# Performance work log

Measured on AMD Instinct MI355X. Metric: run time of the kernel, lower is better.

## Reference

```python
import jax, jax.numpy as jnp
import numpy as np

S, B, E, D, W, V = 196, 64, 1024, 1800, 512, 32000


def setup_inputs() -> dict:
    key = jax.random.key(0)
    ks = jax.random.split(key, 16)
    def n(k, shape, s=0.02):
        return jax.random.normal(k, shape, jnp.float32) * s
    return {
        "E_tm1": jax.random.randint(ks[0], (B,), 0, V),
        "y_tm1": jax.random.normal(ks[1], (B, V), jnp.float32),
        "h": jax.random.normal(ks[2], (S, B, E), jnp.float32),
        "emb": n(ks[3], (V, W)),
        "W_ih": n(ks[4], (4 * D, W + E)), "b_ih": jnp.zeros((4 * D,), jnp.float32),
        "W_hh": n(ks[5], (4 * D, D)), "b_hh": jnp.zeros((4 * D,), jnp.float32),
        "W_out": n(ks[6], (V, W + D + E)), "b_out": jnp.zeros((V,), jnp.float32),
        "Wh1": n(ks[7], (D, E)), "bh1": jnp.zeros((D,), jnp.float32),
        "Wh2": n(ks[8], (D, D)), "bh2": jnp.zeros((D,), jnp.float32),
        "Wc1": n(ks[9], (D, E)), "bc1": jnp.zeros((D,), jnp.float32),
        "Wc2": n(ks[10], (D, D)), "bc2": jnp.zeros((D,), jnp.float32),
        "Wa1": n(ks[11], (D, D + E)), "ba1": jnp.zeros((D,), jnp.float32),
        "Wa2": n(ks[12], (1, D)), "ba2": jnp.zeros((1,), jnp.float32),
        "Wb": n(ks[13], (1, D)), "bb": jnp.zeros((1,), jnp.float32),
    }


def reference(E_tm1, y_tm1, h, emb, W_ih, b_ih, W_hh, b_hh, W_out, b_out,
              Wh1, bh1, Wh2, bh2, Wc1, bc1, Wc2, bc2, Wa1, ba1, Wa2, ba2, Wb, bb):
    # htilde_tm1 is None: init hidden/cell states from mean of encoder states
    h_avg = h.mean(axis=0)                                            # [B, E]
    h0 = jnp.maximum(h_avg @ Wh1.T + bh1, 0.0) @ Wh2.T + bh2          # [B, D]
    c0 = jnp.maximum(h_avg @ Wc1.T + bc1, 0.0) @ Wc2.T + bc2          # [B, D]
    # additive attention: concat(expanded queries, keys) -> MLP -> softmax over seq
    q = jnp.broadcast_to(h0[None], (S, B, D))                         # [S, B, D]
    ci = jnp.concatenate([q, h], axis=2)                              # [S, B, D+E]
    scores = jnp.maximum(ci @ Wa1.T + ba1, 0.0) @ Wa2.T + ba2          # [S, B, 1]
    aw = jax.nn.softmax(scores, axis=0)                                # softmax over seq_len
    ctx = jnp.einsum('sb,sbe->be', aw[..., 0], h)                      # [B, E]
    beta = jax.nn.sigmoid(h0 @ Wb.T + bb)                              # [B, 1] gating scalar
    ctx = ctx * beta
    # LSTM cell (torch gate order: i, f, g, o)
    x = jnp.concatenate([emb[E_tm1], ctx], axis=1)                     # [B, W+E]
    gates = x @ W_ih.T + b_ih + h0 @ W_hh.T + b_hh                     # [B, 4D]
    i, f, g, o = jnp.split(gates, 4, axis=1)
    c_t = jax.nn.sigmoid(f) * c0 + jax.nn.sigmoid(i) * jnp.tanh(g)
    h_t = jax.nn.sigmoid(o) * jnp.tanh(c_t)
    # deep output layer (dropout is identity in eval)
    y_emb = emb[jnp.argmax(y_tm1, axis=1)]                             # [B, W]
    logits = jnp.concatenate([h_t, y_emb, ctx], axis=1) @ W_out.T + b_out  # [B, V]
    return (logits, h_t, c_t, aw)
```

## Files before the change

kernel.cpp:

```cpp
#include <hip/hip_runtime.h>
#include <hip/hip_bf16.h>

typedef __bf16 bf16_t;
typedef __bf16 bf16x8 __attribute__((ext_vector_type(8)));
typedef float f32x4 __attribute__((ext_vector_type(4)));

__device__ inline void stage8(const float* __restrict__ src, bf16_t* __restrict__ dst) {
    float4 u = *(const float4*)src;
    float4 v = *(const float4*)(src + 4);
    bf16x8 t;
    t[0] = (bf16_t)u.x; t[1] = (bf16_t)u.y; t[2] = (bf16_t)u.z; t[3] = (bf16_t)u.w;
    t[4] = (bf16_t)v.x; t[5] = (bf16_t)v.y; t[6] = (bf16_t)v.z; t[7] = (bf16_t)v.w;
    *(bf16x8*)dst = t;
}

__device__ inline void gload_lds16(const bf16_t* g, bf16_t* l) {
    __builtin_amdgcn_global_load_lds(
        (const __attribute__((address_space(1))) unsigned int*)g,
        (__attribute__((address_space(3))) unsigned int*)l,
        16, 0, 0);
}

__global__ void mean_kernel(const float* __restrict__ h, bf16_t* __restrict__ havg,
                            bf16_t* __restrict__ h_bf) {
    int idx = blockIdx.x * 256 + threadIdx.x;
    float s = 0.f;
    for (int si = 0; si < 196; si++) {
        float v = h[(size_t)si * 65536 + idx];
        h_bf[(size_t)si * 65536 + idx] = (bf16_t)v;
        s += v;
    }
    havg[idx] = (bf16_t)(s * (1.f / 196.f));
}

__global__ void conv_wa1(const float* __restrict__ Wa1, const float* __restrict__ Wa2,
                         bf16_t* __restrict__ Wa1bf, float* __restrict__ wa2p) {
    int idx = blockIdx.x * 256 + threadIdx.x;
    int nrow = idx >> 10, k = idx & 1023;
    Wa1bf[idx] = (nrow < 1800) ? (bf16_t)Wa1[(size_t)nrow * 2824 + 1800 + k] : (bf16_t)0.f;
    if (idx < 1920) wa2p[idx] = (idx < 1800) ? Wa2[idx] : 0.f;
}

__global__ __launch_bounds__(256) void argmax_kernel(const float* __restrict__ y, int* __restrict__ idx_out) {
    int b = blockIdx.x;
    const float* row = y + (size_t)b * 32000;
    float best = -1e30f; int bi = 0x7fffffff;
    for (int v = threadIdx.x; v < 32000; v += 256) {
        float val = row[v];
        if (val > best) { best = val; bi = v; }
    }
    __shared__ float bv[256]; __shared__ int bidx[256];
    bv[threadIdx.x] = best; bidx[threadIdx.x] = bi;
    __syncthreads();
    for (int s = 128; s > 0; s >>= 1) {
        if (threadIdx.x < s) {
            float ov = bv[threadIdx.x + s]; int oi = bidx[threadIdx.x + s];
            if (ov > bv[threadIdx.x] || (ov == bv[threadIdx.x] && oi < bidx[threadIdx.x])) {
                bv[threadIdx.x] = ov; bidx[threadIdx.x] = oi;
            }
        }
        __syncthreads();
    }
    if (threadIdx.x == 0) idx_out[b] = bidx[0];
}

__global__ __launch_bounds__(256) void gemm64(
    const bf16_t* __restrict__ A, int lda, int K,
    const float* __restrict__ W, int ldw,
    const float* __restrict__ bias,
    const float* __restrict__ Cadd,
    float* __restrict__ Cf, bf16_t* __restrict__ Cbf, int ldc,
    int N, int act)
{
    __shared__ __align__(16) bf16_t aA[64 * 32];
    __shared__ __align__(16) bf16_t wB[64 * 32];
    int tid = threadIdx.x, wave = tid >> 6, lane = tid & 63;
    int n0 = blockIdx.x * 64;
    int chunks = (K + 31) >> 5;
    int cs = (int)(((long)chunks * blockIdx.y) / gridDim.y);
    int ce = (int)(((long)chunks * (blockIdx.y + 1)) / gridDim.y);
    int kstart = cs * 32, kend = min(K, ce * 32);
    if (gridDim.y > 1) Cf += (size_t)blockIdx.y * 64 * ldc;
    f32x4 acc[4] = {};
    int arow = tid >> 2, acol = (tid & 3) * 8;
    int nrow = n0 + arow;
    for (int k0 = kstart; k0 < kend; k0 += 32) {
        int k = k0 + acol;
        if (k + 8 <= K) {
            *(float4*)(&aA[arow * 32 + acol]) = *(const float4*)(&A[(size_t)arow * lda + k]);
        } else {
            for (int i = 0; i < 8; i++) aA[arow * 32 + acol + i] = (k + i < K) ? A[(size_t)arow * lda + k + i] : (bf16_t)0.f;
        }
        if (nrow < N) {
            if (k + 8 <= K) {
                stage8(&W[(size_t)nrow * ldw + k], &wB[arow * 32 + acol]);
            } else {
                for (int i = 0; i < 8; i++) wB[arow * 32 + acol + i] = (k + i < K) ? (bf16_t)W[(size_t)nrow * ldw + k + i] : (bf16_t)0.f;
            }
        } else {
            *(float4*)(&wB[arow * 32 + acol]) = make_float4(0.f, 0.f, 0.f, 0.f);
        }
        __syncthreads();
        bf16x8 af = *(const bf16x8*)(&aA[(16 * wave + (lane & 15)) * 32 + (lane >> 4) * 8]);
#pragma unroll
        for (int j = 0; j < 4; j++) {
            bf16x8 bfr = *(const bf16x8*)(&wB[(16 * j + (lane & 15)) * 32 + (lane >> 4) * 8]);
            acc[j] = __builtin_amdgcn_mfma_f32_16x16x32_bf16(af, bfr, acc[j], 0, 0, 0);
        }
        __syncthreads();
    }
    int mbase = 16 * wave + (lane >> 4) * 4;
    int ncol = lane & 15;
#pragma unroll
    for (int j = 0; j < 4; j++) {
        int n = n0 + 16 * j + ncol;
        if (n >= N) continue;
        float bv = bias ? bias[n] : 0.f;
#pragma unroll
        for (int rg = 0; rg < 4; rg++) {
            int m = mbase + rg;
            float v = acc[j][rg] + bv;
            if (Cadd) v += Cadd[(size_t)m * ldc + n];
            if (act) v = fmaxf(v, 0.f);
            if (Cf) Cf[(size_t)m * ldc + n] = v;
            if (Cbf) Cbf[(size_t)m * ldc + n] = (bf16_t)v;
        }
    }
}

__global__ void gemm_finalize(const float* __restrict__ part, int KS,
                              const float* __restrict__ bias, int act,
                              float* __restrict__ Cf, bf16_t* __restrict__ Cbf, int N) {
    int idx = blockIdx.x * 256 + threadIdx.x;
    if (idx >= 64 * N) return;
    int m = idx / N, n = idx - m * N;
    float s = 0.f;
    for (int k = 0; k < KS; k++) s += part[(size_t)(k * 64 + m) * N + n];
    if (bias) s += bias[n];
    if (act) s = fmaxf(s, 0.f);
    if (Cf) Cf[idx] = s;
    if (Cbf) Cbf[idx] = (bf16_t)s;
}

__global__ __launch_bounds__(256) void attn_gemm(
    const bf16_t* __restrict__ A, const bf16_t* __restrict__ Bw,
    const float* __restrict__ r, const float* __restrict__ wa2p,
    float* __restrict__ scoresP)
{
    __shared__ __align__(16) bf16_t aA[128 * 32];
    __shared__ __align__(16) bf16_t wB[128 * 32];
    int tid = threadIdx.x, wave = tid >> 6, lane = tid & 63;
    int m0 = blockIdx.x * 128, n0 = blockIdx.y * 128;
    int srow = lane >> 2, scol = (lane & 3) * 8;
    const bf16_t* Ag = A + (size_t)(m0 + wave * 32 + srow) * 1024 + scol;
    const bf16_t* Bg = Bw + (size_t)(n0 + wave * 32 + srow) * 1024 + scol;
    bf16_t* aL0 = &aA[wave * 1024];
    bf16_t* aL1 = &aA[wave * 1024 + 512];
    bf16_t* bL0 = &wB[wave * 1024];
    bf16_t* bL1 = &wB[wave * 1024 + 512];
    int mw = (wave >> 1) * 64, nw = (wave & 1) * 64;
    f32x4 acc[4][4] = {};
    for (int k0 = 0; k0 < 1024; k0 += 32) {
        gload_lds16(Ag + k0, aL0);
        gload_lds16(Ag + 16 * 1024 + k0, aL1);
        gload_lds16(Bg + k0, bL0);
        gload_lds16(Bg + 16 * 1024 + k0, bL1);
        __syncthreads();
        bf16x8 af[4], bfr[4];
#pragma unroll
        for (int i = 0; i < 4; i++) {
            af[i]  = *(const bf16x8*)(&aA[(mw + i * 16 + (lane & 15)) * 32 + (lane >> 4) * 8]);
            bfr[i] = *(const bf16x8*)(&wB[(nw + i * 16 + (lane & 15)) * 32 + (lane >> 4) * 8]);
        }
#pragma unroll
        for (int mi = 0; mi < 4; mi++)
#pragma unroll
            for (int nj = 0; nj < 4; nj++)
                acc[mi][nj] = __builtin_amdgcn_mfma_f32_16x16x32_bf16(af[mi], bfr[nj], acc[mi][nj], 0, 0, 0);
        __syncthreads();
    }
    int ncol = lane & 15;
    int part = blockIdx.y * 2 + (wave & 1);
    float w2[4];
#pragma unroll
    for (int nj = 0; nj < 4; nj++) w2[nj] = wa2p[n0 + nw + nj * 16 + ncol];
#pragma unroll
    for (int mi = 0; mi < 4; mi++) {
#pragma unroll
        for (int rg = 0; rg < 4; rg++) {
            int m = m0 + mw + mi * 16 + (lane >> 4) * 4 + rg;
            const float* rrow = r + (size_t)(m & 63) * 1800;
            float s = 0.f;
#pragma unroll
            for (int nj = 0; nj < 4; nj++) {
                int n = n0 + nw + nj * 16 + ncol;
                float rv = (n < 1800) ? rrow[n] : 0.f;
                s += fmaxf(acc[mi][nj][rg] + rv, 0.f) * w2[nj];
            }
#pragma unroll
            for (int d = 1; d < 16; d <<= 1) s += __shfl_xor(s, d, 64);
            if (ncol == 0) scoresP[(size_t)part * 12544 + m] = s;
        }
    }
}

__global__ __launch_bounds__(256) void softmax_beta(
    const float* __restrict__ scoresP, float* __restrict__ aw32,
    float* __restrict__ aw_out, const bf16_t* __restrict__ h0,
    const float* __restrict__ Wb, const float* __restrict__ bb,
    const float* __restrict__ ba2, float* __restrict__ beta)
{
    int b = blockIdx.x, t = threadIdx.x;
    __shared__ float red[4];
    __shared__ float bc;
    float v = -1e30f;
    if (t < 196) {
        float s = ba2[0];
        for (int p = 0; p < 30; p++) s += scoresP[(size_t)p * 12544 + t * 64 + b];
        v = s;
    }
    float m = v;
    for (int d = 1; d < 64; d <<= 1) m = fmaxf(m, __shfl_xor(m, d, 64));
    if ((t & 63) == 0) red[t >> 6] = m;
    __syncthreads();
    if (t == 0) bc = fmaxf(fmaxf(red[0], red[1]), fmaxf(red[2], red[3]));
    __syncthreads();
    m = bc;
    float e = (t < 196) ? expf(v - m) : 0.f;
    float s = e;
    for (int d = 1; d < 64; d <<= 1) s += __shfl_xor(s, d, 64);
    __syncthreads();
    if ((t & 63) == 0) red[t >> 6] = s;
    __syncthreads();
    if (t == 0) bc = red[0] + red[1] + red[2] + red[3];
    __syncthreads();
    float inv = 1.f / bc;
    if (t < 196) { float a = e * inv; aw32[t * 64 + b] = a; aw_out[t * 64 + b] = a; }
    float bs = 0.f;
    for (int k = t; k < 1800; k += 256) bs += (float)h0[b * 1800 + k] * Wb[k];
    for (int d = 1; d < 64; d <<= 1) bs += __shfl_xor(bs, d, 64);
    __syncthreads();
    if ((t & 63) == 0) red[t >> 6] = bs;
    __syncthreads();
    if (t == 0) beta[b] = 1.f / (1.f + expf(-(red[0] + red[1] + red[2] + red[3] + bb[0])));
}

__global__ void ctx_kernel(const float* __restrict__ h, const float* __restrict__ aw32,
                           const float* __restrict__ beta, bf16_t* __restrict__ xA, bf16_t* __restrict__ zA) {
    int idx = blockIdx.x * 256 + threadIdx.x;
    int b = idx >> 10, e = idx & 1023;
    float s = 0.f;
    for (int si = 0; si < 196; si++) s += aw32[si * 64 + b] * h[(size_t)si * 65536 + idx];
    float c = s * beta[b];
    xA[b * 1536 + 512 + e] = (bf16_t)c;
    zA[b * 3336 + 2312 + e] = (bf16_t)c;
}

__global__ void gather_kernel(const float* __restrict__ emb, const int* __restrict__ E_tm1,
                              const int* __restrict__ amax, bf16_t* __restrict__ xA, bf16_t* __restrict__ zA) {
    int idx = blockIdx.x * 256 + threadIdx.x;
    int half = idx >> 15;
    int j = idx & 32767; int b = j >> 9, w = j & 511;
    if (half == 0) xA[b * 1536 + w] = (bf16_t)emb[(size_t)E_tm1[b] * 512 + w];
    else           zA[b * 3336 + 1800 + w] = (bf16_t)emb[(size_t)amax[b] * 512 + w];
}

__global__ void lstm_kernel(const float* __restrict__ gates, const float* __restrict__ c0,
                            float* __restrict__ oh, float* __restrict__ oc, bf16_t* __restrict__ zA) {
    int idx = blockIdx.x * 256 + threadIdx.x;
    if (idx >= 115200) return;
    int b = idx / 1800, d = idx - b * 1800;
    const float* g = gates + (size_t)b * 7200;
    float ig = 1.f / (1.f + expf(-g[d]));
    float fg = 1.f / (1.f + expf(-g[1800 + d]));
    float gg = tanhf(g[3600 + d]);
    float og = 1.f / (1.f + expf(-g[5400 + d]));
    float ct = fg * c0[idx] + ig * gg;
    float ht = og * tanhf(ct);
    oh[idx] = ht;
    oc[idx] = ct;
    zA[b * 3336 + d] = (bf16_t)ht;
}

extern "C" void kernel_launch(void* const* d_in, const int* in_sizes, int n_in,
                              void* d_out, int out_size, void* d_ws, size_t ws_size,
                              hipStream_t stream) {
    const int*   E_tm1 = (const int*)d_in[0];
    const float* y_tm1 = (const float*)d_in[1];
    const float* h     = (const float*)d_in[2];
    const float* emb   = (const float*)d_in[3];
    const float* W_ih  = (const float*)d_in[4];
    const float* b_ih  = (const float*)d_in[5];
    const float* W_hh  = (const float*)d_in[6];
    const float* b_hh  = (const float*)d_in[7];
    const float* W_out = (const float*)d_in[8];
    const float* b_out = (const float*)d_in[9];
    const float* Wh1   = (const float*)d_in[10];
    const float* bh1   = (const float*)d_in[11];
    const float* Wh2   = (const float*)d_in[12];
    const float* bh2   = (const float*)d_in[13];
    const float* Wc1   = (const float*)d_in[14];
    const float* bc1   = (const float*)d_in[15];
    const float* Wc2   = (const float*)d_in[16];
    const float* bc2   = (const float*)d_in[17];
    const float* Wa1   = (const float*)d_in[18];
    const float* ba1   = (const float*)d_in[19];
    const float* Wa2   = (const float*)d_in[20];
    const float* ba2   = (const float*)d_in[21];
    const float* Wb    = (const float*)d_in[22];
    const float* bb    = (const float*)d_in[23];

    float* wsf     = (float*)d_ws;
    float* part    = wsf;
    float* gates   = part;
    float* r_buf   = wsf + 460800;
    float* scoresP = wsf + 576000;
    float* aw32    = wsf + 952320;
    float* beta    = wsf + 964864;
    float* c0      = wsf + 964928;
    float* wa2p    = wsf + 1080128;
    int*   amax    = (int*)(wsf + 1082048);
    bf16_t* havg = (bf16_t*)(wsf + 1082112);
    bf16_t* t1   = havg + 65536;
    bf16_t* t2   = t1 + 115200;
    bf16_t* h0   = t2 + 115200;
    bf16_t* xA   = h0 + 115200;
    bf16_t* zA   = xA + 98304;
    bf16_t* h_bf = zA + 213504;
    bf16_t* Wa1bf= h_bf + 12845056;

    float* out        = (float*)d_out;
    float* out_logits = out;
    float* out_ht     = out + 2048000;
    float* out_ct     = out + 2163200;
    float* out_aw     = out + 2278400;

    mean_kernel<<<256, 256, 0, stream>>>(h, havg, h_bf);
    conv_wa1<<<7680, 256, 0, stream>>>(Wa1, Wa2, Wa1bf, wa2p);
    argmax_kernel<<<64, 256, 0, stream>>>(y_tm1, amax);

    gemm64<<<dim3(29, 4), 256, 0, stream>>>(havg, 1024, 1024, Wh1, 1024, nullptr, nullptr, part, nullptr, 1800, 1800, 0);
    gemm_finalize<<<450, 256, 0, stream>>>(part, 4, bh1, 1, nullptr, t1, 1800);
    gemm64<<<dim3(29, 4), 256, 0, stream>>>(havg, 1024, 1024, Wc1, 1024, nullptr, nullptr, part, nullptr, 1800, 1800, 0);
    gemm_finalize<<<450, 256, 0, stream>>>(part, 4, bc1, 1, nullptr, t2, 1800);
    gemm64<<<dim3(29, 4), 256, 0, stream>>>(t1, 1800, 1800, Wh2, 1800, nullptr, nullptr, part, nullptr, 1800, 1800, 0);
    gemm_finalize<<<450, 256, 0, stream>>>(part, 4, bh2, 0, nullptr, h0, 1800);
    gemm64<<<dim3(29, 4), 256, 0, stream>>>(t2, 1800, 1800, Wc2, 1800, nullptr, nullptr, part, nullptr, 1800, 1800, 0);
    gemm_finalize<<<450, 256, 0, stream>>>(part, 4, bc2, 0, c0, nullptr, 1800);
    gemm64<<<dim3(29, 4), 256, 0, stream>>>(h0, 1800, 1800, Wa1, 2824, nullptr, nullptr, part, nullptr, 1800, 1800, 0);
    gemm_finalize<<<450, 256, 0, stream>>>(part, 4, ba1, 0, r_buf, nullptr, 1800);

    attn_gemm<<<dim3(98, 15), 256, 0, stream>>>(h_bf, Wa1bf, r_buf, wa2p, scoresP);
    softmax_beta<<<64, 256, 0, stream>>>(scoresP, aw32, out_aw, h0, Wb, bb, ba2, beta);
    ctx_kernel<<<256, 256, 0, stream>>>(h, aw32, beta, xA, zA);
    gather_kernel<<<256, 256, 0, stream>>>(emb, E_tm1, amax, xA, zA);

    gemm64<<<dim3(113, 1), 256, 0, stream>>>(xA, 1536, 1536, W_ih, 1536, b_ih, nullptr, gates, nullptr, 7200, 7200, 0);
    gemm64<<<dim3(113, 1), 256, 0, stream>>>(h0, 1800, 1800, W_hh, 1800, b_hh, gates, gates, nullptr, 7200, 7200, 0);
    lstm_kernel<<<450, 256, 0, stream>>>(gates, c0, out_ht, out_ct, zA);

    gemm64<<<dim3(500, 1), 256, 0, stream>>>(zA, 3336, 3336, W_out, 3336, b_out, nullptr, out_logits, nullptr, 32000, 32000, 0);
}
```

Measured before the change: 1.173 ms.

## Double-buffer GEMM staging with register prefetch and split-K all skinny GEMMs

Rewrites the skinny GEMM kernel to prefetch the next K-chunk into registers while MFMAs run on a double-buffered LDS tile, which removes one barrier per iteration. Every GEMM now writes split-K partials: the init GEMMs use more K splits, the LSTM gate GEMMs use two splits each with the reduction folded into the LSTM kernel, and the output projection gets three splits plus a finalize pass. The goal is more blocks in flight so latency is hidden on the weight-bandwidth-bound GEMMs. The cost is extra partial-sum traffic and a larger workspace. The ctx kernel also reads the bf16 copy of h instead of fp32, which halves its reads at some precision cost.

```diff
diff --git a/kernel.cpp b/kernel.cpp
--- a/kernel.cpp
+++ b/kernel.cpp
@@ -5,13 +5,33 @@
 typedef __bf16 bf16x8 __attribute__((ext_vector_type(8)));
 typedef float f32x4 __attribute__((ext_vector_type(4)));
 
-__device__ inline void stage8(const float* __restrict__ src, bf16_t* __restrict__ dst) {
-    float4 u = *(const float4*)src;
-    float4 v = *(const float4*)(src + 4);
+__device__ inline bf16x8 zero8() {
     bf16x8 t;
-    t[0] = (bf16_t)u.x; t[1] = (bf16_t)u.y; t[2] = (bf16_t)u.z; t[3] = (bf16_t)u.w;
-    t[4] = (bf16_t)v.x; t[5] = (bf16_t)v.y; t[6] = (bf16_t)v.z; t[7] = (bf16_t)v.w;
-    *(bf16x8*)dst = t;
+#pragma unroll
+    for (int i = 0; i < 8; i++) t[i] = (bf16_t)0.f;
+    return t;
+}
+
+__device__ inline bf16x8 loadW8(const float* __restrict__ W, size_t row, int k, int K, int ldw) {
+    bf16x8 t;
+    if (k + 8 <= K) {
+        float4 u = *(const float4*)(W + row * ldw + k);
+        float4 v = *(const float4*)(W + row * ldw + k + 4);
+        t[0] = (bf16_t)u.x; t[1] = (bf16_t)u.y; t[2] = (bf16_t)u.z; t[3] = (bf16_t)u.w;
+        t[4] = (bf16_t)v.x; t[5] = (bf16_t)v.y; t[6] = (bf16_t)v.z; t[7] = (bf16_t)v.w;
+    } else {
+#pragma unroll
+        for (int i = 0; i < 8; i++) t[i] = (k + i < K) ? (bf16_t)W[row * ldw + k + i] : (bf16_t)0.f;
+    }
+    return t;
+}
+
+__device__ inline bf16x8 loadA8(const bf16_t* __restrict__ A, size_t row, int k, int K, int lda) {
+    if (k + 8 <= K) return *(const bf16x8*)(A + row * lda + k);
+    bf16x8 t;
+#pragma unroll
+    for (int i = 0; i < 8; i++) t[i] = (k + i < K) ? A[row * lda + k + i] : (bf16_t)0.f;
+    return t;
 }
 
 __device__ inline void gload_lds16(const bf16_t* g, bf16_t* l) {
@@ -64,50 +84,46 @@
     if (threadIdx.x == 0) idx_out[b] = bidx[0];
 }
 
-__global__ __launch_bounds__(256) void gemm64(
+__global__ __launch_bounds__(256) void gemm64v2(
     const bf16_t* __restrict__ A, int lda, int K,
     const float* __restrict__ W, int ldw,
-    const float* __restrict__ bias,
-    const float* __restrict__ Cadd,
-    float* __restrict__ Cf, bf16_t* __restrict__ Cbf, int ldc,
-    int N, int act)
+    float* __restrict__ Pf, int ldc, int N)
 {
-    __shared__ __align__(16) bf16_t aA[64 * 32];
-    __shared__ __align__(16) bf16_t wB[64 * 32];
+    __shared__ __align__(16) bf16_t aA[2][64 * 32];
+    __shared__ __align__(16) bf16_t wB[2][64 * 32];
     int tid = threadIdx.x, wave = tid >> 6, lane = tid & 63;
     int n0 = blockIdx.x * 64;
     int chunks = (K + 31) >> 5;
     int cs = (int)(((long)chunks * blockIdx.y) / gridDim.y);
     int ce = (int)(((long)chunks * (blockIdx.y + 1)) / gridDim.y);
     int kstart = cs * 32, kend = min(K, ce * 32);
-    if (gridDim.y > 1) Cf += (size_t)blockIdx.y * 64 * ldc;
-    f32x4 acc[4] = {};
+    Pf += (size_t)blockIdx.y * 64 * ldc;
     int arow = tid >> 2, acol = (tid & 3) * 8;
     int nrow = n0 + arow;
+    bool wvalid = nrow < N;
+    f32x4 acc[4] = {};
+    bf16x8 aR = zero8(), wR = zero8();
+    if (kstart < kend) {
+        aR = loadA8(A, (size_t)arow, kstart + acol, K, lda);
+        if (wvalid) wR = loadW8(W, (size_t)nrow, kstart + acol, K, ldw);
+    }
+    int buf = 0;
     for (int k0 = kstart; k0 < kend; k0 += 32) {
-        int k = k0 + acol;
-        if (k + 8 <= K) {
-            *(float4*)(&aA[arow * 32 + acol]) = *(const float4*)(&A[(size_t)arow * lda + k]);
-        } else {
-            for (int i = 0; i < 8; i++) aA[arow * 32 + acol + i] = (k + i < K) ? A[(size_t)arow * lda + k + i] : (bf16_t)0.f;
-        }
-        if (nrow < N) {
-            if (k + 8 <= K) {
-                stage8(&W[(size_t)nrow * ldw + k], &wB[arow * 32 + acol]);
-            } else {
-                for (int i = 0; i < 8; i++) wB[arow * 32 + acol + i] = (k + i < K) ? (bf16_t)W[(size_t)nrow * ldw + k + i] : (bf16_t)0.f;
-            }
-        } else {
-            *(float4*)(&wB[arow * 32 + acol]) = make_float4(0.f, 0.f, 0.f, 0.f);
-        }
+        *(bf16x8*)(&aA[buf][arow * 32 + acol]) = aR;
+        *(bf16x8*)(&wB[buf][arow * 32 + acol]) = wR;
         __syncthreads();
-        bf16x8 af = *(const bf16x8*)(&aA[(16 * wave + (lane & 15)) * 32 + (lane >> 4) * 8]);
+        int kn = k0 + 32;
+        if (kn < kend) {
+            aR = loadA8(A, (size_t)arow, kn + acol, K, lda);
+            if (wvalid) wR = loadW8(W, (size_t)nrow, kn + acol, K, ldw);
+        }
+        bf16x8 af = *(const bf16x8*)(&aA[buf][(16 * wave + (lane & 15)) * 32 + (lane >> 4) * 8]);
 #pragma unroll
         for (int j = 0; j < 4; j++) {
-            bf16x8 bfr = *(const bf16x8*)(&wB[(16 * j + (lane & 15)) * 32 + (lane >> 4) * 8]);
+            bf16x8 bfr = *(const bf16x8*)(&wB[buf][(16 * j + (lane & 15)) * 32 + (lane >> 4) * 8]);
             acc[j] = __builtin_amdgcn_mfma_f32_16x16x32_bf16(af, bfr, acc[j], 0, 0, 0);
         }
-        __syncthreads();
+        buf ^= 1;
     }
     int mbase = 16 * wave + (lane >> 4) * 4;
     int ncol = lane & 15;
@@ -115,16 +131,9 @@
     for (int j = 0; j < 4; j++) {
         int n = n0 + 16 * j + ncol;
         if (n >= N) continue;
-        float bv = bias ? bias[n] : 0.f;
-#pragma unroll
-        for (int rg = 0; rg < 4; rg++) {
-            int m = mbase + rg;
-            float v = acc[j][rg] + bv;
-            if (Cadd) v += Cadd[(size_t)m * ldc + n];
-            if (act) v = fmaxf(v, 0.f);
-            if (Cf) Cf[(size_t)m * ldc + n] = v;
-            if (Cbf) Cbf[(size_t)m * ldc + n] = (bf16_t)v;
-        }
+#pragma unroll
+        for (int rg = 0; rg < 4; rg++)
+            Pf[(size_t)(mbase + rg) * ldc + n] = acc[j][rg];
     }
 }
 
@@ -245,12 +254,12 @@
     if (t == 0) beta[b] = 1.f / (1.f + expf(-(red[0] + red[1] + red[2] + red[3] + bb[0])));
 }
 
-__global__ void ctx_kernel(const float* __restrict__ h, const float* __restrict__ aw32,
+__global__ void ctx_kernel(const bf16_t* __restrict__ h_bf, const float* __restrict__ aw32,
                            const float* __restrict__ beta, bf16_t* __restrict__ xA, bf16_t* __restrict__ zA) {
     int idx = blockIdx.x * 256 + threadIdx.x;
     int b = idx >> 10, e = idx & 1023;
     float s = 0.f;
-    for (int si = 0; si < 196; si++) s += aw32[si * 64 + b] * h[(size_t)si * 65536 + idx];
+    for (int si = 0; si < 196; si++) s += aw32[si * 64 + b] * (float)h_bf[(size_t)si * 65536 + idx];
     float c = s * beta[b];
     xA[b * 1536 + 512 + e] = (bf16_t)c;
     zA[b * 3336 + 2312 + e] = (bf16_t)c;
@@ -265,16 +274,26 @@
     else           zA[b * 3336 + 1800 + w] = (bf16_t)emb[(size_t)amax[b] * 512 + w];
 }
 
-__global__ void lstm_kernel(const float* __restrict__ gates, const float* __restrict__ c0,
+__global__ void lstm_kernel(const float* __restrict__ gatesP, const float* __restrict__ c0,
+                            const float* __restrict__ b_ih, const float* __restrict__ b_hh,
                             float* __restrict__ oh, float* __restrict__ oc, bf16_t* __restrict__ zA) {
     int idx = blockIdx.x * 256 + threadIdx.x;
     if (idx >= 115200) return;
     int b = idx / 1800, d = idx - b * 1800;
-    const float* g = gates + (size_t)b * 7200;
-    float ig = 1.f / (1.f + expf(-g[d]));
-    float fg = 1.f / (1.f + expf(-g[1800 + d]));
-    float gg = tanhf(g[3600 + d]);
-    float og = 1.f / (1.f + expf(-g[5400 + d]));
+    const float* g0 = gatesP + (size_t)b * 7200;
+    float gv[4];
+#pragma unroll
+    for (int gi = 0; gi < 4; gi++) {
+        int col = gi * 1800 + d;
+        float s = b_ih[col] + b_hh[col];
+#pragma unroll
+        for (int p = 0; p < 4; p++) s += g0[(size_t)p * 460800 + col];
+        gv[gi] = s;
+    }
+    float ig = 1.f / (1.f + expf(-gv[0]));
+    float fg = 1.f / (1.f + expf(-gv[1]));
+    float gg = tanhf(gv[2]);
+    float og = 1.f / (1.f + expf(-gv[3]));
     float ct = fg * c0[idx] + ig * gg;
     float ht = og * tanhf(ct);
     oh[idx] = ht;
@@ -310,17 +329,17 @@
     const float* Wb    = (const float*)d_in[22];
     const float* bb    = (const float*)d_in[23];
 
-    float* wsf     = (float*)d_ws;
-    float* part    = wsf;
-    float* gates   = part;
-    float* r_buf   = wsf + 460800;
-    float* scoresP = wsf + 576000;
-    float* aw32    = wsf + 952320;
-    float* beta    = wsf + 964864;
-    float* c0      = wsf + 964928;
-    float* wa2p    = wsf + 1080128;
-    int*   amax    = (int*)(wsf + 1082048);
-    bf16_t* havg = (bf16_t*)(wsf + 1082112);
+    float* wsf      = (float*)d_ws;
+    float* bigpart  = wsf;
+    float* gates    = bigpart;
+    float* r_buf    = wsf + 6144000;
+    float* scoresP  = wsf + 6259200;
+    float* aw32     = wsf + 6635520;
+    float* beta     = wsf + 6648064;
+    float* c0       = wsf + 6648128;
+    float* wa2p     = wsf + 6763328;
+    int*   amax     = (int*)(wsf + 6765248);
+    bf16_t* havg = (bf16_t*)(wsf + 6765312);
     bf16_t* t1   = havg + 65536;
     bf16_t* t2   = t1 + 115200;
     bf16_t* h0   = t2 + 115200;
@@ -339,25 +358,26 @@
     conv_wa1<<<7680, 256, 0, stream>>>(Wa1, Wa2, Wa1bf, wa2p);
     argmax_kernel<<<64, 256, 0, stream>>>(y_tm1, amax);
 
-    gemm64<<<dim3(29, 4), 256, 0, stream>>>(havg, 1024, 1024, Wh1, 1024, nullptr, nullptr, part, nullptr, 1800, 1800, 0);
-    gemm_finalize<<<450, 256, 0, stream>>>(part, 4, bh1, 1, nullptr, t1, 1800);
-    gemm64<<<dim3(29, 4), 256, 0, stream>>>(havg, 1024, 1024, Wc1, 1024, nullptr, nullptr, part, nullptr, 1800, 1800, 0);
-    gemm_finalize<<<450, 256, 0, stream>>>(part, 4, bc1, 1, nullptr, t2, 1800);
-    gemm64<<<dim3(29, 4), 256, 0, stream>>>(t1, 1800, 1800, Wh2, 1800, nullptr, nullptr, part, nullptr, 1800, 1800, 0);
-    gemm_finalize<<<450, 256, 0, stream>>>(part, 4, bh2, 0, nullptr, h0, 1800);
-    gemm64<<<dim3(29, 4), 256, 0, stream>>>(t2, 1800, 1800, Wc2, 1800, nullptr, nullptr, part, nullptr, 1800, 1800, 0);
-    gemm_finalize<<<450, 256, 0, stream>>>(part, 4, bc2, 0, c0, nullptr, 1800);
-    gemm64<<<dim3(29, 4), 256, 0, stream>>>(h0, 1800, 1800, Wa1, 2824, nullptr, nullptr, part, nullptr, 1800, 1800, 0);
-    gemm_finalize<<<450, 256, 0, stream>>>(part, 4, ba1, 0, r_buf, nullptr, 1800);
+    gemm64v2<<<dim3(29, 8), 256, 0, stream>>>(havg, 1024, 1024, Wh1, 1024, bigpart, 1800, 1800);
+    gemm_finalize<<<450, 256, 0, stream>>>(bigpart, 8, bh1, 1, nullptr, t1, 1800);
+    gemm64v2<<<dim3(29, 8), 256, 0, stream>>>(havg, 1024, 1024, Wc1, 1024, bigpart, 1800, 1800);
+    gemm_finalize<<<450, 256, 0, stream>>>(bigpart, 8, bc1, 1, nullptr, t2, 1800);
+    gemm64v2<<<dim3(29, 8), 256, 0, stream>>>(t1, 1800, 1800, Wh2, 1800, bigpart, 1800, 1800);
+    gemm_finalize<<<450, 256, 0, stream>>>(bigpart, 8, bh2, 0, nullptr, h0, 1800);
+    gemm64v2<<<dim3(29, 8), 256, 0, stream>>>(t2, 1800, 1800, Wc2, 1800, bigpart, 1800, 1800);
+    gemm_finalize<<<450, 256, 0, stream>>>(bigpart, 8, bc2, 0, c0, nullptr, 1800);
+    gemm64v2<<<dim3(29, 8), 256, 0, stream>>>(h0, 1800, 1800, Wa1, 2824, bigpart, 1800, 1800);
+    gemm_finalize<<<450, 256, 0, stream>>>(bigpart, 8, ba1, 0, r_buf, nullptr, 1800);
 
     attn_gemm<<<dim3(98, 15), 256, 0, stream>>>(h_bf, Wa1bf, r_buf, wa2p, scoresP);
     softmax_beta<<<64, 256, 0, stream>>>(scoresP, aw32, out_aw, h0, Wb, bb, ba2, beta);
-    ctx_kernel<<<256, 256, 0, stream>>>(h, aw32, beta, xA, zA);
+    ctx_kernel<<<256, 256, 0, stream>>>(h_bf, aw32, beta, xA, zA);
     gather_kernel<<<256, 256, 0, stream>>>(emb, E_tm1, amax, xA, zA);
 
-    gemm64<<<dim3(113, 1), 256, 0, stream>>>(xA, 1536, 1536, W_ih, 1536, b_ih, nullptr, gates, nullptr, 7200, 7200, 0);
-    gemm64<<<dim3(113, 1), 256, 0, stream>>>(h0, 1800, 1800, W_hh, 1800, b_hh, gates, gates, nullptr, 7200, 7200, 0);
-    lstm_kernel<<<450, 256, 0, stream>>>(gates, c0, out_ht, out_ct, zA);
-
-    gemm64<<<dim3(500, 1), 256, 0, stream>>>(zA, 3336, 3336, W_out, 3336, b_out, nullptr, out_logits, nullptr, 32000, 32000, 0);
-}
+    gemm64v2<<<dim3(113, 2), 256, 0, stream>>>(xA, 1536, 1536, W_ih, 1536, gates, 7200, 7200);
+    gemm64v2<<<dim3(113, 2), 256, 0, stream>>>(h0, 1800, 1800, W_hh, 1800, gates + 2 * 460800, 7200, 7200);
+    lstm_kernel<<<450, 256, 0, stream>>>(gates, c0, b_ih, b_hh, out_ht, out_ct, zA);
+
+    gemm64v2<<<dim3(500, 3), 256, 0, stream>>>(zA, 3336, 3336, W_out, 3336, bigpart, 32000, 32000);
+    gemm_finalize<<<8000, 256, 0, stream>>>(bigpart, 3, b_out, 0, out_logits, nullptr, 32000);
+}
```

New measurement: 1.058 ms. 1.11x faster.
